# Performance work log

Hardware: AMD Instinct MI355X
Metric: run time of the kernel (lower is better)

## Reference

```python
import jax, jax.numpy as jnp
import numpy as np

N_HEAD = 8
D_MODEL = 512
D_HEAD = D_MODEL // N_HEAD
D_HIDDEN = 2048
LN_EPS = 1e-5


def setup_inputs() -> dict:
    key = jax.random.key(0)
    ks = jax.random.split(key, 13)
    s = 0.02
    return {
        "spatial_features": jax.random.normal(ks[0], (4096, 64, D_MODEL), dtype=jnp.float32),
        "Wk": jax.random.normal(ks[1], (D_MODEL, D_MODEL), dtype=jnp.float32) * s,
        "bk": jnp.zeros((D_MODEL,), dtype=jnp.float32),
        "Wv": jax.random.normal(ks[2], (D_MODEL, D_MODEL), dtype=jnp.float32) * s,
        "bv": jnp.zeros((D_MODEL,), dtype=jnp.float32),
        "score_w": jax.random.normal(ks[3], (N_HEAD, D_HEAD), dtype=jnp.float32) * s,
        "score_b": jnp.zeros((N_HEAD,), dtype=jnp.float32),
        "W1": jax.random.normal(ks[4], (D_MODEL, D_HIDDEN), dtype=jnp.float32) * s,
        "b1": jnp.zeros((D_HIDDEN,), dtype=jnp.float32),
        "W2": jax.random.normal(ks[5], (D_HIDDEN, D_MODEL), dtype=jnp.float32) * s,
        "b2": jnp.zeros((D_MODEL,), dtype=jnp.float32),
        "ln_g": jnp.ones((D_MODEL,), dtype=jnp.float32),
        "ln_b": jnp.zeros((D_MODEL,), dtype=jnp.float32),
    }


def reference(spatial_features, Wk, bk, Wv, bv, score_w, score_b,
              W1, b1, W2, b2, ln_g, ln_b):
    B, N, _ = spatial_features.shape
    # k, v projections -> [B, N, H, Dh]
    k = (spatial_features @ Wk + bk).reshape(B, N, N_HEAD, D_HEAD)
    v = (spatial_features @ Wv + bv).reshape(B, N, N_HEAD, D_HEAD)
    # per-head score: Linear(d_head -> 1) batched over heads
    score = jnp.einsum('bnhd,hd->bnh', k, score_w) + score_b  # [B, N, H]
    attn = jax.nn.softmax(score, axis=1)                       # softmax over N
    # weighted sum pooling over N, then concat heads -> [B, d_model]
    feature = jnp.einsum('bnh,bnhd->bhd', attn, v).reshape(B, D_MODEL)
    # FFN with residual + layernorm (dropout = eval identity)
    h = jax.nn.gelu(feature @ W1 + b1, approximate=False)
    y = h @ W2 + b2 + feature
    mu = jnp.mean(y, axis=-1, keepdims=True)
    var = jnp.mean((y - mu) ** 2, axis=-1, keepdims=True)
    out = (y - mu) * jax.lax.rsqrt(var + LN_EPS) * ln_g + ln_b
    return out
```

## Files before the change

kernel.cpp:

```cpp
#include <hip/hip_runtime.h>
#include <hip/hip_bf16.h>

#define N_HEAD 8
#define D_MODEL 512
#define D_HEAD 64
#define D_HIDDEN 2048
#define NTOK 64
#define BATCH 4096

typedef __attribute__((ext_vector_type(4))) float f32x4;
typedef __attribute__((ext_vector_type(8))) short short8;
typedef __attribute__((ext_vector_type(8))) unsigned short u16x8;
typedef __attribute__((ext_vector_type(4))) unsigned short u16x4;

__device__ __forceinline__ float bf2f(unsigned short u) {
    return __uint_as_float(((unsigned int)u) << 16);
}
__device__ __forceinline__ unsigned short f2bf(float f) {
    unsigned int b = __float_as_uint(f);
    b += 0x7fffu + ((b >> 16) & 1u);
    return (unsigned short)(b >> 16);
}
__device__ __forceinline__ float wave_sum(float v) {
    v += __shfl_xor(v, 32); v += __shfl_xor(v, 16); v += __shfl_xor(v, 8);
    v += __shfl_xor(v, 4);  v += __shfl_xor(v, 2);  v += __shfl_xor(v, 1);
    return v;
}
__device__ __forceinline__ void gload_lds16(const void* g, void* l) {
    __builtin_amdgcn_global_load_lds(
        (const __attribute__((address_space(1))) unsigned int*)g,
        (__attribute__((address_space(3))) unsigned int*)l, 16, 0, 0);
}

__global__ __launch_bounds__(256) void prep_all(
    const float* __restrict__ Wk, const float* __restrict__ score_w,
    const float* __restrict__ Wv, const float* __restrict__ W1,
    const float* __restrict__ W2,
    unsigned short* __restrict__ uT,
    unsigned short* __restrict__ WvT, unsigned short* __restrict__ W1T,
    unsigned short* __restrict__ W2T) {
    int m = blockIdx.y;
    if (m == 3) {
        int idx = blockIdx.x * 256 + threadIdx.x;
        if (idx < 16 * 512) {
            int h = idx & 15, c = idx >> 4;
            float s = 0.f;
            if (h < 8) {
                #pragma unroll 8
                for (int d = 0; d < D_HEAD; ++d)
                    s += Wk[c * D_MODEL + h * D_HEAD + d] * score_w[h * D_HEAD + d];
            }
            uT[h * D_MODEL + c] = f2bf(s);
        }
        return;
    }
    const float* in; unsigned short* out; int K, N, tX, tiles;
    if (m == 0)      { in = Wv; out = WvT; K = 512;  N = 512;  tX = 16; tiles = 256;  }
    else if (m == 1) { in = W1; out = W1T; K = 512;  N = 2048; tX = 64; tiles = 1024; }
    else             { in = W2; out = W2T; K = 2048; N = 512;  tX = 16; tiles = 1024; }
    int t = blockIdx.x;
    if (t >= tiles) return;
    int n0 = (t % tX) * 32, k0 = (t / tX) * 32;
    __shared__ float tile[32][33];
    int tx = threadIdx.x & 31, ty = threadIdx.x >> 5;
    #pragma unroll
    for (int i = ty; i < 32; i += 8)
        tile[i][tx] = in[(size_t)(k0 + i) * N + n0 + tx];
    __syncthreads();
    #pragma unroll
    for (int i = ty; i < 32; i += 8)
        out[(size_t)(n0 + i) * K + k0 + tx] = f2bf(tile[tx][i]);
}

__global__ __launch_bounds__(256) void score_pool_v11(
    const float* __restrict__ x, const unsigned short* __restrict__ uT,
    unsigned short* __restrict__ pooled) {
    __shared__ unsigned short xl[16 * D_MODEL];
    __shared__ unsigned short ul[8 * D_MODEL];
    __shared__ float el[16 * 8];
    __shared__ float zacc[8];

    const int tid = threadIdx.x;
    const int l = tid & 63, w = tid >> 6;
    const int hg = l >> 4, lr = l & 15;

    {
        int r = tid >> 5;
        int c16 = (tid & 31) * 16;
        u16x8 v0 = *(const u16x8*)(uT + r * D_MODEL + c16);
        u16x8 v1 = *(const u16x8*)(uT + r * D_MODEL + c16 + 8);
        *(u16x8*)&ul[r * D_MODEL + ((c16) ^ (r << 3))] = v0;
        *(u16x8*)&ul[r * D_MODEL + ((c16 + 8) ^ (r << 3))] = v1;
    }

    const int trow = tid >> 7;
    const int col4 = (tid & 127) * 4;

    const int o8 = (tid & 63) * 8;
    const int hp = tid >> 6;

    const int b0 = blockIdx.x * 4;

    float4 pre[8];
    {
        const float4* p = (const float4*)(x + (size_t)b0 * (NTOK * D_MODEL));
        #pragma unroll
        for (int j = 0; j < 8; ++j) pre[j] = p[j * 256 + tid];
    }

    float acc[16];
    #pragma unroll
    for (int k = 0; k < 16; ++k) acc[k] = 0.f;

    #pragma unroll 1
    for (int qq = 0; qq < 16; ++qq) {
        const int q = qq & 3;
        if (q == 0 && tid < 8) zacc[tid] = 0.f;
        #pragma unroll
        for (int j = 0; j < 8; ++j) {
            int row = 2 * j + trow;
            float4 a = pre[j];
            u16x4 ov = {f2bf(a.x), f2bf(a.y), f2bf(a.z), f2bf(a.w)};
            *(u16x4*)&xl[row * D_MODEL + (col4 ^ ((row & 7) << 3))] = ov;
        }
        if (qq < 15) {
            const int nb = b0 + ((qq + 1) >> 2), nq = (qq + 1) & 3;
            const float4* p = (const float4*)(x + (size_t)nb * (NTOK * D_MODEL) +
                                              nq * 16 * D_MODEL);
            #pragma unroll
            for (int j = 0; j < 8; ++j) pre[j] = p[j * 256 + tid];
        }
        asm volatile("s_waitcnt lgkmcnt(0)" ::: "memory");
        __builtin_amdgcn_s_barrier();

        if (w == q) {
            f32x4 sacc = {0.f, 0.f, 0.f, 0.f};
            const int rbase = lr * D_MODEL;
            const int rsw = (lr & 7) << 3;
            #pragma unroll
            for (int ks = 0; ks < 16; ++ks) {
                int off = ks * 32 + hg * 8;
                short8 uf;
                if (lr < 8) uf = *(const short8*)&ul[lr * D_MODEL + (off ^ (lr << 3))];
                else        uf = (short8){0, 0, 0, 0, 0, 0, 0, 0};
                short8 xf = *(const short8*)&xl[rbase + (off ^ rsw)];
                sacc = __builtin_amdgcn_mfma_f32_16x16x32_bf16(uf, xf, sacc, 0, 0, 0);
            }
            f32x4 ev;
            float zsum[4];
            #pragma unroll
            for (int j = 0; j < 4; ++j) {
                float e = __expf(sacc[j]);
                ev[j] = e;
                e += __shfl_xor(e, 1); e += __shfl_xor(e, 2);
                e += __shfl_xor(e, 4); e += __shfl_xor(e, 8);
                zsum[j] = e;
            }
            if (hg < 2) {
                *(f32x4*)&el[lr * 8 + hg * 4] = ev;
                if (lr == 0) {
                    f32x4 z = *(const f32x4*)&zacc[hg * 4];
                    z[0] += zsum[0]; z[1] += zsum[1];
                    z[2] += zsum[2]; z[3] += zsum[3];
                    *(f32x4*)&zacc[hg * 4] = z;
                }
            }
        }
        asm volatile("s_waitcnt lgkmcnt(0)" ::: "memory");
        __builtin_amdgcn_s_barrier();

        #pragma unroll 4
        for (int t = 0; t < 16; ++t) {
            u16x8 xr = *(const u16x8*)&xl[t * D_MODEL + (o8 ^ ((t & 7) << 3))];
            float2 e2 = *(const float2*)&el[t * 8 + hp * 2];
            #pragma unroll
            for (int cc = 0; cc < 8; ++cc) {
                float xf = bf2f(xr[cc]);
                acc[cc]     += e2.x * xf;
                acc[8 + cc] += e2.y * xf;
            }
        }
        if (q == 3) {
            float2 za = *(const float2*)&zacc[hp * 2];
            float r0 = 1.f / za.x, r1 = 1.f / za.y;
            unsigned short* pb = pooled + (size_t)(b0 + (qq >> 2)) * (N_HEAD * D_MODEL);
            u16x8 o0, o1;
            #pragma unroll
            for (int cc = 0; cc < 8; ++cc) {
                o0[cc] = f2bf(acc[cc] * r0);
                o1[cc] = f2bf(acc[8 + cc] * r1);
            }
            *(u16x8*)&pb[(hp * 2) * D_MODEL + o8] = o0;
            *(u16x8*)&pb[(hp * 2 + 1) * D_MODEL + o8] = o1;
            #pragma unroll
            for (int k = 0; k < 16; ++k) acc[k] = 0.f;
        }
        asm volatile("s_waitcnt lgkmcnt(0)" ::: "memory");
        __builtin_amdgcn_s_barrier();
    }
}

template <int BM, int BN, int MODE>
__global__ __launch_bounds__(256) void gemm_mf(
    const unsigned short* __restrict__ A, int lda,
    const unsigned short* __restrict__ BT,
    const float* __restrict__ bias,
    void* __restrict__ Cout, int ldc,
    const unsigned short* __restrict__ res, int K) {
    __shared__ unsigned short Al[BM * 64];
    __shared__ unsigned short Bl[BN * 64];
    int m0 = blockIdx.x * BM;
    int n0;
    const unsigned short* Ap = A;
    const unsigned short* Bp;
    const float* bp;
    if (MODE == 0) {
        int h = blockIdx.y;
        Ap = A + (size_t)h * 512;
        Bp = BT + (size_t)h * 64 * K;
        bp = bias + h * 64;
        n0 = h * 64;
    } else {
        n0 = blockIdx.y * BN;
        Bp = BT + (size_t)n0 * K;
        bp = bias + n0;
    }
    int tid = threadIdx.x, l = tid & 63, w = tid >> 6;
    int lr = l & 15, lq = l >> 4;
    int wm = w >> 1, wn = w & 1;
    constexpr int MR = BM / 32, NR = BN / 32;
    constexpr int AI = BM / 8, BI = BN / 8;

    f32x4 acc[MR][NR];
    #pragma unroll
    for (int mi = 0; mi < MR; ++mi)
        #pragma unroll
        for (int nj = 0; nj < NR; ++nj) acc[mi][nj] = (f32x4){0.f, 0.f, 0.f, 0.f};

    int srow = l >> 3;
    int scol = ((l & 7) ^ ((l >> 3) & 7)) << 3;

    for (int k0 = 0; k0 < K; k0 += 64) {
        #pragma unroll
        for (int j = 0; j < AI / 4; ++j) {
            int ji = w * (AI / 4) + j;
            const unsigned short* src = Ap + (size_t)(m0 + ji * 8 + srow) * lda + k0 + scol;
            gload_lds16(src, &Al[ji * 512]);
        }
        #pragma unroll
        for (int j = 0; j < BI / 4; ++j) {
            int ji = w * (BI / 4) + j;
            const unsigned short* src = Bp + (size_t)(ji * 8 + srow) * K + k0 + scol;
            gload_lds16(src, &Bl[ji * 512]);
        }
        __syncthreads();
        #pragma unroll
        for (int kk = 0; kk < 64; kk += 32) {
            int sw = (kk + lq * 8) ^ ((l & 7) << 3);
            short8 af[MR], bf[NR];
            #pragma unroll
            for (int mi = 0; mi < MR; ++mi)
                af[mi] = *(const short8*)&Al[(wm * (BM / 2) + mi * 16 + lr) * 64 + sw];
            #pragma unroll
            for (int nj = 0; nj < NR; ++nj)
                bf[nj] = *(const short8*)&Bl[(wn * (BN / 2) + nj * 16 + lr) * 64 + sw];
            #pragma unroll
            for (int mi = 0; mi < MR; ++mi)
                #pragma unroll
                for (int nj = 0; nj < NR; ++nj)
                    acc[mi][nj] = __builtin_amdgcn_mfma_f32_16x16x32_bf16(
                        af[mi], bf[nj], acc[mi][nj], 0, 0, 0);
        }
        __syncthreads();
    }

    #pragma unroll
    for (int mi = 0; mi < MR; ++mi) {
        #pragma unroll
        for (int nj = 0; nj < NR; ++nj) {
            #pragma unroll
            for (int j = 0; j < 4; ++j) {
                int row = m0 + wm * (BM / 2) + mi * 16 + lq * 4 + j;
                int nl = wn * (BN / 2) + nj * 16 + lr;
                int col = n0 + nl;
                float v = acc[mi][nj][j] + bp[nl];
                if (MODE == 1) {
                    v = 0.5f * v * (1.0f + erff(v * 0.70710678118654752f));
                }
                if (MODE == 2) {
                    v += bf2f(res[(size_t)row * 512 + col]);
                    ((float*)Cout)[(size_t)row * ldc + col] = v;
                } else {
                    ((unsigned short*)Cout)[(size_t)row * ldc + col] = f2bf(v);
                }
            }
        }
    }
}

__global__ __launch_bounds__(256) void ln_kernel(
    float* __restrict__ y, const float* __restrict__ g, const float* __restrict__ bta) {
    int row = blockIdx.x * 4 + (threadIdx.x >> 6);
    int l = threadIdx.x & 63;
    float* yp = y + (size_t)row * D_MODEL;
    float4 v0 = *(const float4*)(yp + l * 8);
    float4 v1 = *(const float4*)(yp + l * 8 + 4);
    float vv[8] = {v0.x, v0.y, v0.z, v0.w, v1.x, v1.y, v1.z, v1.w};
    float s = 0.f;
    #pragma unroll
    for (int i = 0; i < 8; ++i) s += vv[i];
    s = wave_sum(s);
    float mean = s * (1.f / 512.f);
    float q = 0.f;
    #pragma unroll
    for (int i = 0; i < 8; ++i) { float d = vv[i] - mean; q += d * d; }
    q = wave_sum(q);
    float rstd = rsqrtf(q * (1.f / 512.f) + 1e-5f);
    float4 g0 = *(const float4*)(g + l * 8);
    float4 g1 = *(const float4*)(g + l * 8 + 4);
    float4 b0 = *(const float4*)(bta + l * 8);
    float4 b1 = *(const float4*)(bta + l * 8 + 4);
    float gv[8] = {g0.x, g0.y, g0.z, g0.w, g1.x, g1.y, g1.z, g1.w};
    float bv[8] = {b0.x, b0.y, b0.z, b0.w, b1.x, b1.y, b1.z, b1.w};
    float ov[8];
    #pragma unroll
    for (int i = 0; i < 8; ++i) ov[i] = (vv[i] - mean) * rstd * gv[i] + bv[i];
    float4 o0 = {ov[0], ov[1], ov[2], ov[3]};
    float4 o1 = {ov[4], ov[5], ov[6], ov[7]};
    *(float4*)(yp + l * 8) = o0;
    *(float4*)(yp + l * 8 + 4) = o1;
}

extern "C" void kernel_launch(void* const* d_in, const int* in_sizes, int n_in,
                              void* d_out, int out_size, void* d_ws, size_t ws_size,
                              hipStream_t stream) {
    const float* x       = (const float*)d_in[0];
    const float* Wk      = (const float*)d_in[1];
    const float* Wv      = (const float*)d_in[3];
    const float* bv      = (const float*)d_in[4];
    const float* score_w = (const float*)d_in[5];
    const float* W1      = (const float*)d_in[7];
    const float* b1      = (const float*)d_in[8];
    const float* W2      = (const float*)d_in[9];
    const float* b2      = (const float*)d_in[10];
    const float* ln_g    = (const float*)d_in[11];
    const float* ln_b    = (const float*)d_in[12];
    float* out = (float*)d_out;

    char* ws = (char*)d_ws;
    size_t off = 0;
    auto alloc = [&](size_t sz) {
        void* p = ws + off;
        off = (off + sz + 1023) & ~(size_t)1023;
        return p;
    };
    unsigned short* uT  = (unsigned short*)alloc((size_t)16 * D_MODEL * 2);
    unsigned short* WvT = (unsigned short*)alloc((size_t)512 * 512 * 2);
    unsigned short* W1T = (unsigned short*)alloc((size_t)2048 * 512 * 2);
    unsigned short* W2T = (unsigned short*)alloc((size_t)512 * 2048 * 2);
    unsigned short* pooled = (unsigned short*)alloc((size_t)BATCH * N_HEAD * D_MODEL * 2);
    unsigned short* feat   = (unsigned short*)alloc((size_t)BATCH * D_MODEL * 2);
    unsigned short* Hbuf   = (unsigned short*)alloc((size_t)BATCH * D_HIDDEN * 2);

    prep_all<<<dim3(1024, 4), dim3(256), 0, stream>>>(
        Wk, score_w, Wv, W1, W2, uT, WvT, W1T, W2T);
    score_pool_v11<<<dim3(1024), dim3(256), 0, stream>>>(x, uT, pooled);
    gemm_mf<128, 64, 0><<<dim3(32, 8), dim3(256), 0, stream>>>(
        pooled, N_HEAD * D_MODEL, WvT, bv, (void*)feat, D_MODEL,
        (const unsigned short*)nullptr, 512);
    gemm_mf<128, 128, 1><<<dim3(32, 16), dim3(256), 0, stream>>>(
        feat, D_MODEL, W1T, b1, (void*)Hbuf, D_HIDDEN,
        (const unsigned short*)nullptr, 512);
    gemm_mf<64, 128, 2><<<dim3(64, 4), dim3(256), 0, stream>>>(
        Hbuf, D_HIDDEN, W2T, b2, (void*)out, D_MODEL, feat, 2048);
    ln_kernel<<<dim3(1024), dim3(256), 0, stream>>>(out, ln_g, ln_b);
}
```

Baseline: 215.2 us.

## Pool from fp32 registers with double-buffered prefetch, dropping per-quarter barrier

The pooling kernel now accumulates the softmax-weighted sum directly from the fp32 values already held in registers, not by re-reading the bf16 tile from LDS. It ping-pongs two register prefetch buffers via a lambda and removes the trailing barrier on non-final quarters. Each thread owns 4 columns by 8 heads for its half of the rows, and the two halves are reduced through LDS scratch at batch end. This cuts LDS traffic and bf16 rounding in pooling, but doubles prefetch registers and the accumulator to 32, which raises register pressure under the launch bound of 4 blocks.

```diff
diff --git a/kernel.cpp b/kernel.cpp
--- a/kernel.cpp
+++ b/kernel.cpp
@@ -72,7 +72,7 @@
         out[(size_t)(n0 + i) * K + k0 + tx] = f2bf(tile[tx][i]);
 }
 
-__global__ __launch_bounds__(256) void score_pool_v11(
+__global__ __launch_bounds__(256, 4) void score_pool_v12(
     const float* __restrict__ x, const unsigned short* __restrict__ uT,
     unsigned short* __restrict__ pooled) {
     __shared__ unsigned short xl[16 * D_MODEL];
@@ -95,31 +95,26 @@
 
     const int trow = tid >> 7;
     const int col4 = (tid & 127) * 4;
-
-    const int o8 = (tid & 63) * 8;
-    const int hp = tid >> 6;
-
     const int b0 = blockIdx.x * 4;
 
-    float4 pre[8];
+    float4 preA[8], preB[8];
     {
         const float4* p = (const float4*)(x + (size_t)b0 * (NTOK * D_MODEL));
         #pragma unroll
-        for (int j = 0; j < 8; ++j) pre[j] = p[j * 256 + tid];
-    }
-
-    float acc[16];
-    #pragma unroll
-    for (int k = 0; k < 16; ++k) acc[k] = 0.f;
-
-    #pragma unroll 1
-    for (int qq = 0; qq < 16; ++qq) {
+        for (int j = 0; j < 8; ++j) preA[j] = p[j * 256 + tid];
+    }
+
+    float acc[32];
+    #pragma unroll
+    for (int k = 0; k < 32; ++k) acc[k] = 0.f;
+
+    auto quarter = [&](float4 (&cur)[8], float4 (&nxt)[8], int qq) {
         const int q = qq & 3;
         if (q == 0 && tid < 8) zacc[tid] = 0.f;
         #pragma unroll
         for (int j = 0; j < 8; ++j) {
             int row = 2 * j + trow;
-            float4 a = pre[j];
+            float4 a = cur[j];
             u16x4 ov = {f2bf(a.x), f2bf(a.y), f2bf(a.z), f2bf(a.w)};
             *(u16x4*)&xl[row * D_MODEL + (col4 ^ ((row & 7) << 3))] = ov;
         }
@@ -128,7 +123,7 @@
             const float4* p = (const float4*)(x + (size_t)nb * (NTOK * D_MODEL) +
                                               nq * 16 * D_MODEL);
             #pragma unroll
-            for (int j = 0; j < 8; ++j) pre[j] = p[j * 256 + tid];
+            for (int j = 0; j < 8; ++j) nxt[j] = p[j * 256 + tid];
         }
         asm volatile("s_waitcnt lgkmcnt(0)" ::: "memory");
         __builtin_amdgcn_s_barrier();
@@ -169,34 +164,76 @@
         asm volatile("s_waitcnt lgkmcnt(0)" ::: "memory");
         __builtin_amdgcn_s_barrier();
 
-        #pragma unroll 4
-        for (int t = 0; t < 16; ++t) {
-            u16x8 xr = *(const u16x8*)&xl[t * D_MODEL + (o8 ^ ((t & 7) << 3))];
-            float2 e2 = *(const float2*)&el[t * 8 + hp * 2];
-            #pragma unroll
-            for (int cc = 0; cc < 8; ++cc) {
-                float xf = bf2f(xr[cc]);
-                acc[cc]     += e2.x * xf;
-                acc[8 + cc] += e2.y * xf;
-            }
-        }
+        #pragma unroll
+        for (int j = 0; j < 8; ++j) {
+            int t = 2 * j + trow;
+            f32x4 e0 = *(const f32x4*)&el[t * 8];
+            f32x4 e1 = *(const f32x4*)&el[t * 8 + 4];
+            float xc[4] = {cur[j].x, cur[j].y, cur[j].z, cur[j].w};
+            #pragma unroll
+            for (int c = 0; c < 4; ++c) {
+                float xv = xc[c];
+                acc[c * 8 + 0] += e0[0] * xv;
+                acc[c * 8 + 1] += e0[1] * xv;
+                acc[c * 8 + 2] += e0[2] * xv;
+                acc[c * 8 + 3] += e0[3] * xv;
+                acc[c * 8 + 4] += e1[0] * xv;
+                acc[c * 8 + 5] += e1[1] * xv;
+                acc[c * 8 + 6] += e1[2] * xv;
+                acc[c * 8 + 7] += e1[3] * xv;
+            }
+        }
+
         if (q == 3) {
-            float2 za = *(const float2*)&zacc[hp * 2];
-            float r0 = 1.f / za.x, r1 = 1.f / za.y;
-            unsigned short* pb = pooled + (size_t)(b0 + (qq >> 2)) * (N_HEAD * D_MODEL);
-            u16x8 o0, o1;
-            #pragma unroll
-            for (int cc = 0; cc < 8; ++cc) {
-                o0[cc] = f2bf(acc[cc] * r0);
-                o1[cc] = f2bf(acc[8 + cc] * r1);
-            }
-            *(u16x8*)&pb[(hp * 2) * D_MODEL + o8] = o0;
-            *(u16x8*)&pb[(hp * 2 + 1) * D_MODEL + o8] = o1;
-            #pragma unroll
-            for (int k = 0; k < 16; ++k) acc[k] = 0.f;
-        }
-        asm volatile("s_waitcnt lgkmcnt(0)" ::: "memory");
-        __builtin_amdgcn_s_barrier();
+            float* scr = (float*)xl;
+            const int s = tid & 127;
+            const int sw4 = (s & 7) << 2;
+            if (trow) {
+                #pragma unroll
+                for (int k = 0; k < 8; ++k) {
+                    f32x4 v = {acc[k * 4], acc[k * 4 + 1], acc[k * 4 + 2], acc[k * 4 + 3]};
+                    *(f32x4*)&scr[s * 32 + ((k * 4) ^ sw4)] = v;
+                }
+            }
+            asm volatile("s_waitcnt lgkmcnt(0)" ::: "memory");
+            __builtin_amdgcn_s_barrier();
+            if (!trow) {
+                #pragma unroll
+                for (int k = 0; k < 8; ++k) {
+                    f32x4 v = *(const f32x4*)&scr[s * 32 + ((k * 4) ^ sw4)];
+                    acc[k * 4] += v[0]; acc[k * 4 + 1] += v[1];
+                    acc[k * 4 + 2] += v[2]; acc[k * 4 + 3] += v[3];
+                }
+                f32x4 z0 = *(const f32x4*)&zacc[0];
+                f32x4 z1 = *(const f32x4*)&zacc[4];
+                float rz[8];
+                #pragma unroll
+                for (int h = 0; h < 4; ++h) {
+                    rz[h] = 1.f / z0[h];
+                    rz[4 + h] = 1.f / z1[h];
+                }
+                unsigned short* pb = pooled +
+                    (size_t)(b0 + (qq >> 2)) * (N_HEAD * D_MODEL);
+                #pragma unroll
+                for (int h = 0; h < 8; ++h) {
+                    u16x4 o = {f2bf(acc[0 * 8 + h] * rz[h]),
+                               f2bf(acc[1 * 8 + h] * rz[h]),
+                               f2bf(acc[2 * 8 + h] * rz[h]),
+                               f2bf(acc[3 * 8 + h] * rz[h])};
+                    *(u16x4*)&pb[h * D_MODEL + col4] = o;
+                }
+            }
+            #pragma unroll
+            for (int k = 0; k < 32; ++k) acc[k] = 0.f;
+            asm volatile("s_waitcnt lgkmcnt(0)" ::: "memory");
+            __builtin_amdgcn_s_barrier();
+        }
+    };
+
+    #pragma unroll 1
+    for (int it = 0; it < 8; ++it) {
+        quarter(preA, preB, 2 * it);
+        quarter(preB, preA, 2 * it + 1);
     }
 }
 
@@ -364,7 +401,7 @@
 
     prep_all<<<dim3(1024, 4), dim3(256), 0, stream>>>(
         Wk, score_w, Wv, W1, W2, uT, WvT, W1T, W2T);
-    score_pool_v11<<<dim3(1024), dim3(256), 0, stream>>>(x, uT, pooled);
+    score_pool_v12<<<dim3(1024), dim3(256), 0, stream>>>(x, uT, pooled);
     gemm_mf<128, 64, 0><<<dim3(32, 8), dim3(256), 0, stream>>>(
         pooled, N_HEAD * D_MODEL, WvT, bv, (void*)feat, D_MODEL,
         (const unsigned short*)nullptr, 512);
```

Result: slower. 752.8 us (+249.8%).

## Pool from fp32 registers with double-buffered prefetch and two batches per block

Applied to the files above, without the earlier changes.

The score/pool kernel now handles 2 batches per block over a grid of 2048 instead of 4 batches over 1024. It double-buffers the register prefetch of x (preA/preB) so the next chunk's loads no longer overwrite the registers still in use. The weighted pooling now reads the fp32 values straight from registers instead of re-reading the bf16 copy from LDS, and the two row halves are combined through an LDS scratch reduction. This aims to cut LDS traffic and bf16 rounding in pooling and to give more blocks for occupancy, at the cost of more registers and an extra barrier per batch.

```diff
diff --git a/kernel.cpp b/kernel.cpp
--- a/kernel.cpp
+++ b/kernel.cpp
@@ -72,7 +72,7 @@
         out[(size_t)(n0 + i) * K + k0 + tx] = f2bf(tile[tx][i]);
 }
 
-__global__ __launch_bounds__(256) void score_pool_v11(
+__global__ __launch_bounds__(256) void score_pool_v13(
     const float* __restrict__ x, const unsigned short* __restrict__ uT,
     unsigned short* __restrict__ pooled) {
     __shared__ unsigned short xl[16 * D_MODEL];
@@ -95,109 +95,147 @@
 
     const int trow = tid >> 7;
     const int col4 = (tid & 127) * 4;
-
-    const int o8 = (tid & 63) * 8;
-    const int hp = tid >> 6;
-
-    const int b0 = blockIdx.x * 4;
-
-    float4 pre[8];
+    const int b0 = blockIdx.x * 2;
+
+    float4 preA[8], preB[8];
+    f32x4 acc[4][2];
+    #pragma unroll
+    for (int c = 0; c < 4; ++c) {
+        acc[c][0] = (f32x4){0.f, 0.f, 0.f, 0.f};
+        acc[c][1] = (f32x4){0.f, 0.f, 0.f, 0.f};
+    }
+
     {
         const float4* p = (const float4*)(x + (size_t)b0 * (NTOK * D_MODEL));
         #pragma unroll
-        for (int j = 0; j < 8; ++j) pre[j] = p[j * 256 + tid];
-    }
-
-    float acc[16];
-    #pragma unroll
-    for (int k = 0; k < 16; ++k) acc[k] = 0.f;
+        for (int j = 0; j < 8; ++j) preA[j] = p[j * 256 + tid];
+    }
+
+    int qq = 0;
+
+#define QBODY(CUR, NXT)                                                        \
+    {                                                                          \
+        const int q = qq & 3;                                                  \
+        if (q == 0 && tid < 8) zacc[tid] = 0.f;                                \
+        _Pragma("unroll")                                                      \
+        for (int j = 0; j < 8; ++j) {                                          \
+            int row = 2 * j + trow;                                            \
+            float4 a = CUR[j];                                                 \
+            u16x4 ov = {f2bf(a.x), f2bf(a.y), f2bf(a.z), f2bf(a.w)};           \
+            *(u16x4*)&xl[row * D_MODEL + (col4 ^ ((row & 7) << 3))] = ov;      \
+        }                                                                      \
+        if (qq < 7) {                                                          \
+            const int nb = b0 + ((qq + 1) >> 2), nq = (qq + 1) & 3;            \
+            const float4* p = (const float4*)(x +                              \
+                (size_t)nb * (NTOK * D_MODEL) + nq * 16 * D_MODEL);            \
+            _Pragma("unroll")                                                  \
+            for (int j = 0; j < 8; ++j) NXT[j] = p[j * 256 + tid];             \
+        }                                                                      \
+        asm volatile("s_waitcnt lgkmcnt(0)" ::: "memory");                     \
+        __builtin_amdgcn_s_barrier();                                   \
+        if (w == q) {                                                          \
+            f32x4 sacc = {0.f, 0.f, 0.f, 0.f};                                 \
+            const int rbase = lr * D_MODEL;                                    \
+            const int rsw = (lr & 7) << 3;                                     \
+            _Pragma("unroll")                                                  \
+            for (int ks = 0; ks < 16; ++ks) {                                  \
+                int off = ks * 32 + hg * 8;                                    \
+                short8 uf;                                                     \
+                if (lr < 8) uf = *(const short8*)&ul[lr * D_MODEL +            \
+                                                     (off ^ (lr << 3))];       \
+                else        uf = (short8){0, 0, 0, 0, 0, 0, 0, 0};             \
+                short8 xf = *(const short8*)&xl[rbase + (off ^ rsw)];          \
+                sacc = __builtin_amdgcn_mfma_f32_16x16x32_bf16(uf, xf, sacc,   \
+                                                               0, 0, 0);       \
+            }                                                                  \
+            f32x4 ev;                                                          \
+            float zsum[4];                                                     \
+            _Pragma("unroll")                                                  \
+            for (int j = 0; j < 4; ++j) {                                      \
+                float e = __expf(sacc[j]);                                     \
+                ev[j] = e;                                                     \
+                e += __shfl_xor(e, 1); e += __shfl_xor(e, 2);                  \
+                e += __shfl_xor(e, 4); e += __shfl_xor(e, 8);                  \
+                zsum[j] = e;                                                   \
+            }                                                                  \
+            if (hg < 2) {                                                      \
+                *(f32x4*)&el[lr * 8 + hg * 4] = ev;                            \
+                if (lr == 0) {                                                 \
+                    f32x4 z = *(const f32x4*)&zacc[hg * 4];                    \
+                    z[0] += zsum[0]; z[1] += zsum[1];                          \
+                    z[2] += zsum[2]; z[3] += zsum[3];                          \
+                    *(f32x4*)&zacc[hg * 4] = z;                                \
+                }                                                              \
+            }                                                                  \
+        }                                                                      \
+        asm volatile("s_waitcnt lgkmcnt(0)" ::: "memory");                     \
+        __builtin_amdgcn_s_barrier();                                   \
+        _Pragma("unroll")                                                      \
+        for (int j = 0; j < 8; ++j) {                                          \
+            int t = 2 * j + trow;                                              \
+            f32x4 e0 = *(const f32x4*)&el[t * 8];                              \
+            f32x4 e1 = *(const f32x4*)&el[t * 8 + 4];                          \
+            float4 a = CUR[j];                                                 \
+            acc[0][0] += e0 * a.x; acc[0][1] += e1 * a.x;                      \
+            acc[1][0] += e0 * a.y; acc[1][1] += e1 * a.y;                      \
+            acc[2][0] += e0 * a.z; acc[2][1] += e1 * a.z;                      \
+            acc[3][0] += e0 * a.w; acc[3][1] += e1 * a.w;                      \
+        }                                                                      \
+        if (q == 3) {                                                          \
+            float* scr = (float*)xl;                                           \
+            const int s = tid & 127;                                           \
+            const int sw4 = (s & 7) << 2;                                      \
+            if (trow) {                                                        \
+                _Pragma("unroll")                                              \
+                for (int c = 0; c < 4; ++c) {                                  \
+                    _Pragma("unroll")                                          \
+                    for (int hh = 0; hh < 2; ++hh)                             \
+                        *(f32x4*)&scr[s * 32 +                                 \
+                            (((c * 2 + hh) * 4) ^ sw4)] = acc[c][hh];          \
+                }                                                              \
+            }                                                                  \
+            asm volatile("s_waitcnt lgkmcnt(0)" ::: "memory");                 \
+            __builtin_amdgcn_s_barrier();                              \
+            if (!trow) {                                                       \
+                _Pragma("unroll")                                              \
+                for (int c = 0; c < 4; ++c) {                                  \
+                    _Pragma("unroll")                                          \
+                    for (int hh = 0; hh < 2; ++hh)                             \
+                        acc[c][hh] += *(const f32x4*)&scr[s * 32 +             \
+                            (((c * 2 + hh) * 4) ^ sw4)];                       \
+                }                                                              \
+                f32x4 z0 = *(const f32x4*)&zacc[0];                            \
+                f32x4 z1 = *(const f32x4*)&zacc[4];                            \
+                unsigned short* pb = pooled +                                  \
+                    (size_t)(b0 + (qq >> 2)) * (N_HEAD * D_MODEL);             \
+                _Pragma("unroll")                                              \
+                for (int h = 0; h < 8; ++h) {                                  \
+                    const int hh = h >> 2, hi = h & 3;                         \
+                    float rzh = 1.f / (h < 4 ? z0[hi] : z1[hi]);               \
+                    u16x4 o = {f2bf(acc[0][hh][hi] * rzh),                     \
+                               f2bf(acc[1][hh][hi] * rzh),                     \
+                               f2bf(acc[2][hh][hi] * rzh),                     \
+                               f2bf(acc[3][hh][hi] * rzh)};                    \
+                    *(u16x4*)&pb[h * D_MODEL + col4] = o;                      \
+                }                                                              \
+            }                                                                  \
+            _Pragma("unroll")                                                  \
+            for (int c = 0; c < 4; ++c) {                                      \
+                acc[c][0] = (f32x4){0.f, 0.f, 0.f, 0.f};                       \
+                acc[c][1] = (f32x4){0.f, 0.f, 0.f, 0.f};                       \
+            }                                                                  \
+            asm volatile("s_waitcnt lgkmcnt(0)" ::: "memory");                 \
+            __builtin_amdgcn_s_barrier();                              \
+        }                                                                      \
+        ++qq;                                                                  \
+    }
 
     #pragma unroll 1
-    for (int qq = 0; qq < 16; ++qq) {
-        const int q = qq & 3;
-        if (q == 0 && tid < 8) zacc[tid] = 0.f;
-        #pragma unroll
-        for (int j = 0; j < 8; ++j) {
-            int row = 2 * j + trow;
-            float4 a = pre[j];
-            u16x4 ov = {f2bf(a.x), f2bf(a.y), f2bf(a.z), f2bf(a.w)};
-            *(u16x4*)&xl[row * D_MODEL + (col4 ^ ((row & 7) << 3))] = ov;
-        }
-        if (qq < 15) {
-            const int nb = b0 + ((qq + 1) >> 2), nq = (qq + 1) & 3;
-            const float4* p = (const float4*)(x + (size_t)nb * (NTOK * D_MODEL) +
-                                              nq * 16 * D_MODEL);
-            #pragma unroll
-            for (int j = 0; j < 8; ++j) pre[j] = p[j * 256 + tid];
-        }
-        asm volatile("s_waitcnt lgkmcnt(0)" ::: "memory");
-        __builtin_amdgcn_s_barrier();
-
-        if (w == q) {
-            f32x4 sacc = {0.f, 0.f, 0.f, 0.f};
-            const int rbase = lr * D_MODEL;
-            const int rsw = (lr & 7) << 3;
-            #pragma unroll
-            for (int ks = 0; ks < 16; ++ks) {
-                int off = ks * 32 + hg * 8;
-                short8 uf;
-                if (lr < 8) uf = *(const short8*)&ul[lr * D_MODEL + (off ^ (lr << 3))];
-                else        uf = (short8){0, 0, 0, 0, 0, 0, 0, 0};
-                short8 xf = *(const short8*)&xl[rbase + (off ^ rsw)];
-                sacc = __builtin_amdgcn_mfma_f32_16x16x32_bf16(uf, xf, sacc, 0, 0, 0);
-            }
-            f32x4 ev;
-            float zsum[4];
-            #pragma unroll
-            for (int j = 0; j < 4; ++j) {
-                float e = __expf(sacc[j]);
-                ev[j] = e;
-                e += __shfl_xor(e, 1); e += __shfl_xor(e, 2);
-                e += __shfl_xor(e, 4); e += __shfl_xor(e, 8);
-                zsum[j] = e;
-            }
-            if (hg < 2) {
-                *(f32x4*)&el[lr * 8 + hg * 4] = ev;
-                if (lr == 0) {
-                    f32x4 z = *(const f32x4*)&zacc[hg * 4];
-                    z[0] += zsum[0]; z[1] += zsum[1];
-                    z[2] += zsum[2]; z[3] += zsum[3];
-                    *(f32x4*)&zacc[hg * 4] = z;
-                }
-            }
-        }
-        asm volatile("s_waitcnt lgkmcnt(0)" ::: "memory");
-        __builtin_amdgcn_s_barrier();
-
-        #pragma unroll 4
-        for (int t = 0; t < 16; ++t) {
-            u16x8 xr = *(const u16x8*)&xl[t * D_MODEL + (o8 ^ ((t & 7) << 3))];
-            float2 e2 = *(const float2*)&el[t * 8 + hp * 2];
-            #pragma unroll
-            for (int cc = 0; cc < 8; ++cc) {
-                float xf = bf2f(xr[cc]);
-                acc[cc]     += e2.x * xf;
-                acc[8 + cc] += e2.y * xf;
-            }
-        }
-        if (q == 3) {
-            float2 za = *(const float2*)&zacc[hp * 2];
-            float r0 = 1.f / za.x, r1 = 1.f / za.y;
-            unsigned short* pb = pooled + (size_t)(b0 + (qq >> 2)) * (N_HEAD * D_MODEL);
-            u16x8 o0, o1;
-            #pragma unroll
-            for (int cc = 0; cc < 8; ++cc) {
-                o0[cc] = f2bf(acc[cc] * r0);
-                o1[cc] = f2bf(acc[8 + cc] * r1);
-            }
-            *(u16x8*)&pb[(hp * 2) * D_MODEL + o8] = o0;
-            *(u16x8*)&pb[(hp * 2 + 1) * D_MODEL + o8] = o1;
-            #pragma unroll
-            for (int k = 0; k < 16; ++k) acc[k] = 0.f;
-        }
-        asm volatile("s_waitcnt lgkmcnt(0)" ::: "memory");
-        __builtin_amdgcn_s_barrier();
-    }
+    for (int it = 0; it < 4; ++it) {
+        QBODY(preA, preB)
+        QBODY(preB, preA)
+    }
+#undef QBODY
 }
 
 template <int BM, int BN, int MODE>
@@ -364,7 +402,7 @@
 
     prep_all<<<dim3(1024, 4), dim3(256), 0, stream>>>(
         Wk, score_w, Wv, W1, W2, uT, WvT, W1T, W2T);
-    score_pool_v11<<<dim3(1024), dim3(256), 0, stream>>>(x, uT, pooled);
+    score_pool_v13<<<dim3(2048), dim3(256), 0, stream>>>(x, uT, pooled);
     gemm_mf<128, 64, 0><<<dim3(32, 8), dim3(256), 0, stream>>>(
         pooled, N_HEAD * D_MODEL, WvT, bv, (void*)feat, D_MODEL,
         (const unsigned short*)nullptr, 512);
```

Result: slower. 236.2 us (+9.8%).
